# Kernel tuning notes

Measured on AMD Instinct MI355X. Metric: run time of the kernel, lower is better.

## Reference

```python
import jax, jax.numpy as jnp
import numpy as np

N = 50000
E = 800000
F_IN = 64
HID = 64


def setup_inputs() -> dict:
    key = jax.random.key(0)
    k1, k2, k3, k4, k5, k6 = jax.random.split(key, 6)
    x = jax.random.normal(k1, (N, F_IN), dtype=jnp.float32)
    edge_index = jax.random.randint(k2, (2, E), 0, N, dtype=jnp.int64)
    # GraphSAGE mean-aggregator layers: Linear(2*in -> out) applied to [x || mean_agg(x)]
    W1 = jax.random.normal(k3, (2 * F_IN, HID), dtype=jnp.float32) / np.sqrt(2 * F_IN)
    b1 = jnp.zeros((HID,), dtype=jnp.float32)
    W2 = jax.random.normal(k4, (2 * HID, HID), dtype=jnp.float32) / np.sqrt(2 * HID)
    b2 = jnp.zeros((HID,), dtype=jnp.float32)
    return {"x": x, "edge_index": edge_index, "W1": W1, "b1": b1, "W2": W2, "b2": b2}


def _sage_conv(x, src, dst, W, b):
    # mean aggregation of neighbor (src) features at dst, then linear on [self || agg]
    msg = x[src]                                                   # [E, d] gather
    s = jax.ops.segment_sum(msg, dst, num_segments=N)              # [N, d]
    cnt = jax.ops.segment_sum(jnp.ones((src.shape[0], 1), x.dtype), dst, num_segments=N)
    agg = s / jnp.maximum(cnt, 1.0)
    return jnp.concatenate([x, agg], axis=-1) @ W + b


def reference(x, edge_index, W1, b1, W2, b2):
    src, dst = edge_index[0], edge_index[1]
    h = _sage_conv(x, src, dst, W1, b1)
    h = jax.nn.relu(h)  # dropout is identity at inference
    h = _sage_conv(h, src, dst, W2, b2)
    return h
```

## Files before the change

### kernel.cpp

```cpp
#include <hip/hip_runtime.h>

#define N_NODES 50000
#define N_EDGES 800000
#define F 64
#define CHUNK 6144
#define NWG1 ((N_EDGES + CHUNK - 1) / CHUNK)
#define NBUCK 196
#define BSTRIDE 8192
#define NWTILE (N_NODES / 16)

typedef __attribute__((ext_vector_type(8))) _Float16 half8;
typedef __attribute__((ext_vector_type(4))) float f32x4;

__global__ __launch_bounds__(256) void partition_conv(
    const int*    __restrict__ src, const int* __restrict__ dst,
    const float4* __restrict__ xin,
    half8*        __restrict__ x16,
    const float*  __restrict__ W1, const float* __restrict__ W2,
    _Float16*     __restrict__ Wt1, _Float16* __restrict__ Wt2,
    unsigned*     __restrict__ bcur,
    unsigned*     __restrict__ ebuf) {
  int t = threadIdx.x, b = blockIdx.x;
  if (b == NWG1) {
    for (int i = t; i < 64 * 128; i += 256) {
      int n = i >> 7, k = i & 127;
      Wt1[i] = (_Float16)W1[k * 64 + n];
      Wt2[i] = (_Float16)W2[k * 64 + n];
    }
    return;
  }
  __shared__ int hist[256], lscan[256], lcur[256], gbase[256];
  __shared__ unsigned stage[CHUNK];
  hist[t] = 0; __syncthreads();
  int e0 = b * CHUNK;
  int cnt = N_EDGES - e0; if (cnt > CHUNK) cnt = CHUNK;
  for (int i = t; i < cnt; i += 256) atomicAdd(&hist[dst[e0 + i] >> 8], 1);

  const int TOT = N_NODES * F / 8;
  for (int i = b * 256 + t; i < TOT; i += NWG1 * 256) {
    float4 a = xin[i * 2], c = xin[i * 2 + 1];
    half8 hh;
    hh[0] = (_Float16)a.x; hh[1] = (_Float16)a.y;
    hh[2] = (_Float16)a.z; hh[3] = (_Float16)a.w;
    hh[4] = (_Float16)c.x; hh[5] = (_Float16)c.y;
    hh[6] = (_Float16)c.z; hh[7] = (_Float16)c.w;
    x16[i] = hh;
  }
  __syncthreads();

  int v = hist[t];
  lscan[t] = v; __syncthreads();
  for (int off = 1; off < 256; off <<= 1) {
    int a = (t >= off) ? lscan[t - off] : 0;
    __syncthreads();
    lscan[t] += a;
    __syncthreads();
  }
  lscan[t] -= v;
  lcur[t] = lscan[t];
  if (v > 0) gbase[t] = (int)atomicAdd(&bcur[t], (unsigned)v);
  __syncthreads();

  for (int i = t; i < cnt; i += 256) {
    int d = dst[e0 + i], s = src[e0 + i];
    int bb = d >> 8;
    int p = atomicAdd(&lcur[bb], 1);
    stage[p] = ((unsigned)bb << 24) | ((unsigned)(d & 255) << 16) | (unsigned)s;
  }
  __syncthreads();
  for (int i = t; i < cnt; i += 256) {
    unsigned e = stage[i];
    int bb = e >> 24;
    ebuf[bb * BSTRIDE + gbase[bb] + (i - lscan[bb])] = e;
  }
}

__global__ __launch_bounds__(256) void bucket_sort(
    const unsigned* __restrict__ ebuf, const unsigned* __restrict__ bcur,
    unsigned short* __restrict__ edge_src, int* __restrict__ row_start,
    int* __restrict__ deg) {
  __shared__ int lhist[256], lscan[256], lcur[256];
  __shared__ unsigned short srt[BSTRIDE];
  int b = blockIdx.x, t = threadIdx.x;
  int s0 = b * BSTRIDE;
  int cnt = (int)bcur[b];

  lhist[t] = 0; __syncthreads();
  for (int i = t; i < cnt; i += 256) atomicAdd(&lhist[(ebuf[s0 + i] >> 16) & 255], 1);
  __syncthreads();

  int v = lhist[t];
  lscan[t] = v; __syncthreads();
  for (int off = 1; off < 256; off <<= 1) {
    int a = (t >= off) ? lscan[t - off] : 0;
    __syncthreads();
    lscan[t] += a;
    __syncthreads();
  }
  lscan[t] -= v;
  lcur[t] = lscan[t];
  __syncthreads();

  for (int i = t; i < cnt; i += 256) {
    unsigned e = ebuf[s0 + i];
    int p = atomicAdd(&lcur[(e >> 16) & 255], 1);
    srt[p] = (unsigned short)(e & 0xFFFFu);
  }
  __syncthreads();

  for (int i = t; i < cnt; i += 256) edge_src[s0 + i] = srt[i];

  int n = b * 256 + t;
  if (n < N_NODES) { row_start[n] = s0 + lscan[t]; deg[n] = v; }
}

__global__ __launch_bounds__(256) void sage_layer_fused(
    const half8*    __restrict__ feat16,
    const _Float16* __restrict__ self16,
    const int*      __restrict__ row_start,
    const int*      __restrict__ deg,
    const unsigned short* __restrict__ edge_src,
    const _Float16* __restrict__ Wt,
    const float*    __restrict__ bias,
    float*          __restrict__ outf,
    unsigned short* __restrict__ out16,
    int do_relu) {
  __shared__ _Float16 lmean[32 * 72];
  int t = threadIdx.x;
  int w = t >> 6, lane = t & 63;

  {
    int o = lane >> 3, q = lane & 7;
    int n = blockIdx.x * 32 + w * 8 + o;
    if (n < N_NODES) {
      int start = row_start[n];
      int d     = deg[n];
      float a0=0.f,a1=0.f,a2=0.f,a3=0.f,a4=0.f,a5=0.f,a6=0.f,a7=0.f;
      for (int base = 0; base < d; base += 8) {
        #pragma unroll
        for (int uu = 0; uu < 8; ++uu) {
          int e = base + uu;
          if (e < d) {
            int s = (int)edge_src[start + e];
            half8 v = feat16[(size_t)s * 8 + q];
            a0 += (float)v[0]; a1 += (float)v[1]; a2 += (float)v[2]; a3 += (float)v[3];
            a4 += (float)v[4]; a5 += (float)v[5]; a6 += (float)v[6]; a7 += (float)v[7];
          }
        }
      }
      float inv = (d > 0) ? 1.0f / (float)d : 0.0f;
      half8 h;
      h[0] = (_Float16)(a0*inv); h[1] = (_Float16)(a1*inv);
      h[2] = (_Float16)(a2*inv); h[3] = (_Float16)(a3*inv);
      h[4] = (_Float16)(a4*inv); h[5] = (_Float16)(a5*inv);
      h[6] = (_Float16)(a6*inv); h[7] = (_Float16)(a7*inv);
      *(half8*)&lmean[(w * 8 + o) * 72 + q * 8] = h;
    }
  }
  __syncthreads();

  int tile = w >> 1;
  int wt = blockIdx.x * 2 + tile;
  if (wt >= NWTILE) return;
  int m = lane & 15, quad = lane >> 4;
  size_t arow = (size_t)(wt * 16 + m) * 64 + quad * 8;
  half8 a0 = *(const half8*)(self16 + arow);
  half8 a1 = *(const half8*)(self16 + arow + 32);
  int ln = tile * 16 + m;
  half8 a2 = *(const half8*)&lmean[ln * 72 + quad * 8];
  half8 a3 = *(const half8*)&lmean[ln * 72 + quad * 8 + 32];

  int nt0 = (w & 1) * 2;
  #pragma unroll
  for (int i = 0; i < 2; ++i) {
    int nt = nt0 + i;
    float bv = bias[nt * 16 + m];
    f32x4 acc = (f32x4){bv, bv, bv, bv};
    const _Float16* wrow = Wt + (size_t)(nt * 16 + m) * 128 + quad * 8;
    half8 b0 = *(const half8*)(wrow);
    half8 b1 = *(const half8*)(wrow + 32);
    half8 b2 = *(const half8*)(wrow + 64);
    half8 b3 = *(const half8*)(wrow + 96);
    acc = __builtin_amdgcn_mfma_f32_16x16x32_f16(a0, b0, acc, 0, 0, 0);
    acc = __builtin_amdgcn_mfma_f32_16x16x32_f16(a1, b1, acc, 0, 0, 0);
    acc = __builtin_amdgcn_mfma_f32_16x16x32_f16(a2, b2, acc, 0, 0, 0);
    acc = __builtin_amdgcn_mfma_f32_16x16x32_f16(a3, b3, acc, 0, 0, 0);
    #pragma unroll
    for (int r = 0; r < 4; ++r) {
      size_t off = (size_t)(wt * 16 + quad * 4 + r) * 64 + nt * 16 + m;
      float v = acc[r];
      if (do_relu) v = fmaxf(v, 0.0f);
      if (outf)  outf[off] = v;
      if (out16) { _Float16 hv = (_Float16)v; out16[off] = *(unsigned short*)&hv; }
    }
  }
}

extern "C" void kernel_launch(void* const* d_in, const int* in_sizes, int n_in,
                              void* d_out, int out_size, void* d_ws, size_t ws_size,
                              hipStream_t stream) {
  const float* x  = (const float*)d_in[0];
  const int*   ei = (const int*)d_in[1];
  const float* W1 = (const float*)d_in[2];
  const float* b1 = (const float*)d_in[3];
  const float* W2 = (const float*)d_in[4];
  const float* b2 = (const float*)d_in[5];
  float* out = (float*)d_out;

  const int* src = ei;
  const int* dst = ei + N_EDGES;

  int* wsi       = (int*)d_ws;
  unsigned* bcur = (unsigned*)wsi;
  int* deg       = wsi + 256;
  int* row_start = wsi + 50304;
  unsigned short* edge_src = (unsigned short*)(wsi + 100352);
  unsigned* ebuf = (unsigned*)(wsi + 903168);
  half8* x16     = (half8*)(wsi + 2508800);
  unsigned short* h116 = (unsigned short*)(wsi + 4108800);
  _Float16* Wt1  = (_Float16*)(wsi + 5708800);
  _Float16* Wt2  = (_Float16*)(wsi + 5712896);

  hipMemsetAsync(bcur, 0, 256 * sizeof(unsigned), stream);

  dim3 blk(256);
  partition_conv<<<NWG1 + 1, blk, 0, stream>>>(
      src, dst, (const float4*)x, x16, W1, W2, Wt1, Wt2, bcur, ebuf);
  bucket_sort<<<NBUCK, blk, 0, stream>>>(ebuf, bcur, edge_src, row_start, deg);

  dim3 grd_fused((N_NODES + 31) / 32);

  sage_layer_fused<<<grd_fused, blk, 0, stream>>>(
      x16, (const _Float16*)x16, row_start, deg, edge_src,
      Wt1, b1, nullptr, h116, 1);
  sage_layer_fused<<<grd_fused, blk, 0, stream>>>(
      (const half8*)h116, (const _Float16*)h116, row_start, deg, edge_src,
      Wt2, b2, out, nullptr, 0);
}
```

Measured before the change: 160.4 us.

## Split fp16 features into column halves and gather each half in separate passes

The fp16 feature tables are stored as two 32-column halves (lo and hi), 64 bytes per node each. The aggregation gathers all edges for the lo half, then repeats the pass for the hi half, presumably to shrink the working set per pass and improve cache hit rate on random gathers. Accumulation now happens in fp16 half4 vectors instead of fp32 scalars, which cuts conversion work but risks precision loss on high-degree nodes. The edge indices are read twice, and each gather load is narrower (8 bytes per lane instead of 16).

```diff
diff --git a/kernel.cpp b/kernel.cpp
--- a/kernel.cpp
+++ b/kernel.cpp
@@ -10,12 +10,14 @@
 #define NWTILE (N_NODES / 16)
 
 typedef __attribute__((ext_vector_type(8))) _Float16 half8;
+typedef __attribute__((ext_vector_type(4))) _Float16 half4;
 typedef __attribute__((ext_vector_type(4))) float f32x4;
 
 __global__ __launch_bounds__(256) void partition_conv(
     const int*    __restrict__ src, const int* __restrict__ dst,
     const float4* __restrict__ xin,
-    half8*        __restrict__ x16,
+    half8*        __restrict__ xlo8,
+    half8*        __restrict__ xhi8,
     const float*  __restrict__ W1, const float* __restrict__ W2,
     _Float16*     __restrict__ Wt1, _Float16* __restrict__ Wt2,
     unsigned*     __restrict__ bcur,
@@ -44,7 +46,9 @@
     hh[2] = (_Float16)a.z; hh[3] = (_Float16)a.w;
     hh[4] = (_Float16)c.x; hh[5] = (_Float16)c.y;
     hh[6] = (_Float16)c.z; hh[7] = (_Float16)c.w;
-    x16[i] = hh;
+    int node = i >> 3, part = i & 7;
+    if (part < 4) xlo8[node * 4 + part]       = hh;
+    else          xhi8[node * 4 + (part - 4)] = hh;
   }
   __syncthreads();
 
@@ -115,15 +119,18 @@
 }
 
 __global__ __launch_bounds__(256) void sage_layer_fused(
-    const half8*    __restrict__ feat16,
-    const _Float16* __restrict__ self16,
+    const half4*    __restrict__ glo,
+    const half4*    __restrict__ ghi,
+    const _Float16* __restrict__ slo,
+    const _Float16* __restrict__ shi,
     const int*      __restrict__ row_start,
     const int*      __restrict__ deg,
     const unsigned short* __restrict__ edge_src,
     const _Float16* __restrict__ Wt,
     const float*    __restrict__ bias,
     float*          __restrict__ outf,
-    unsigned short* __restrict__ out16,
+    unsigned short* __restrict__ o16lo,
+    unsigned short* __restrict__ o16hi,
     int do_relu) {
   __shared__ _Float16 lmean[32 * 72];
   int t = threadIdx.x;
@@ -135,26 +142,38 @@
     if (n < N_NODES) {
       int start = row_start[n];
       int d     = deg[n];
-      float a0=0.f,a1=0.f,a2=0.f,a3=0.f,a4=0.f,a5=0.f,a6=0.f,a7=0.f;
+      half4 aclo = (half4){0, 0, 0, 0};
+      half4 achi = (half4){0, 0, 0, 0};
       for (int base = 0; base < d; base += 8) {
         #pragma unroll
         for (int uu = 0; uu < 8; ++uu) {
           int e = base + uu;
           if (e < d) {
             int s = (int)edge_src[start + e];
-            half8 v = feat16[(size_t)s * 8 + q];
-            a0 += (float)v[0]; a1 += (float)v[1]; a2 += (float)v[2]; a3 += (float)v[3];
-            a4 += (float)v[4]; a5 += (float)v[5]; a6 += (float)v[6]; a7 += (float)v[7];
+            aclo += glo[(size_t)s * 8 + q];
           }
         }
       }
+      for (int base = 0; base < d; base += 8) {
+        #pragma unroll
+        for (int uu = 0; uu < 8; ++uu) {
+          int e = base + uu;
+          if (e < d) {
+            int s = (int)edge_src[start + e];
+            achi += ghi[(size_t)s * 8 + q];
+          }
+        }
+      }
       float inv = (d > 0) ? 1.0f / (float)d : 0.0f;
-      half8 h;
-      h[0] = (_Float16)(a0*inv); h[1] = (_Float16)(a1*inv);
-      h[2] = (_Float16)(a2*inv); h[3] = (_Float16)(a3*inv);
-      h[4] = (_Float16)(a4*inv); h[5] = (_Float16)(a5*inv);
-      h[6] = (_Float16)(a6*inv); h[7] = (_Float16)(a7*inv);
-      *(half8*)&lmean[(w * 8 + o) * 72 + q * 8] = h;
+      half4 mlo, mhi;
+      #pragma unroll
+      for (int k = 0; k < 4; ++k) {
+        mlo[k] = (_Float16)((float)aclo[k] * inv);
+        mhi[k] = (_Float16)((float)achi[k] * inv);
+      }
+      int ln = w * 8 + o;
+      *(half4*)&lmean[ln * 72 + q * 4]      = mlo;
+      *(half4*)&lmean[ln * 72 + 32 + q * 4] = mhi;
     }
   }
   __syncthreads();
@@ -163,12 +182,12 @@
   int wt = blockIdx.x * 2 + tile;
   if (wt >= NWTILE) return;
   int m = lane & 15, quad = lane >> 4;
-  size_t arow = (size_t)(wt * 16 + m) * 64 + quad * 8;
-  half8 a0 = *(const half8*)(self16 + arow);
-  half8 a1 = *(const half8*)(self16 + arow + 32);
+  size_t srow = (size_t)(wt * 16 + m) * 32 + quad * 8;
+  half8 a0 = *(const half8*)(slo + srow);
+  half8 a1 = *(const half8*)(shi + srow);
   int ln = tile * 16 + m;
   half8 a2 = *(const half8*)&lmean[ln * 72 + quad * 8];
-  half8 a3 = *(const half8*)&lmean[ln * 72 + quad * 8 + 32];
+  half8 a3 = *(const half8*)&lmean[ln * 72 + 32 + quad * 8];
 
   int nt0 = (w & 1) * 2;
   #pragma unroll
@@ -187,11 +206,17 @@
     acc = __builtin_amdgcn_mfma_f32_16x16x32_f16(a3, b3, acc, 0, 0, 0);
     #pragma unroll
     for (int r = 0; r < 4; ++r) {
-      size_t off = (size_t)(wt * 16 + quad * 4 + r) * 64 + nt * 16 + m;
+      size_t row = (size_t)(wt * 16 + quad * 4 + r);
+      int col = nt * 16 + m;
       float v = acc[r];
       if (do_relu) v = fmaxf(v, 0.0f);
-      if (outf)  outf[off] = v;
-      if (out16) { _Float16 hv = (_Float16)v; out16[off] = *(unsigned short*)&hv; }
+      if (outf) outf[row * 64 + col] = v;
+      if (o16lo) {
+        _Float16 hv = (_Float16)v;
+        unsigned short us = *(unsigned short*)&hv;
+        if (nt < 2) o16lo[row * 32 + col] = us;
+        else        o16hi[row * 32 + (col - 32)] = us;
+      }
     }
   }
 }
@@ -216,8 +241,10 @@
   int* row_start = wsi + 50304;
   unsigned short* edge_src = (unsigned short*)(wsi + 100352);
   unsigned* ebuf = (unsigned*)(wsi + 903168);
-  half8* x16     = (half8*)(wsi + 2508800);
-  unsigned short* h116 = (unsigned short*)(wsi + 4108800);
+  _Float16* xlo  = (_Float16*)(wsi + 2508800);
+  _Float16* xhi  = (_Float16*)(wsi + 3308800);
+  _Float16* h1lo = (_Float16*)(wsi + 4108800);
+  _Float16* h1hi = (_Float16*)(wsi + 4908800);
   _Float16* Wt1  = (_Float16*)(wsi + 5708800);
   _Float16* Wt2  = (_Float16*)(wsi + 5712896);
 
@@ -225,15 +252,18 @@
 
   dim3 blk(256);
   partition_conv<<<NWG1 + 1, blk, 0, stream>>>(
-      src, dst, (const float4*)x, x16, W1, W2, Wt1, Wt2, bcur, ebuf);
+      src, dst, (const float4*)x, (half8*)xlo, (half8*)xhi,
+      W1, W2, Wt1, Wt2, bcur, ebuf);
   bucket_sort<<<NBUCK, blk, 0, stream>>>(ebuf, bcur, edge_src, row_start, deg);
 
   dim3 grd_fused((N_NODES + 31) / 32);
 
   sage_layer_fused<<<grd_fused, blk, 0, stream>>>(
-      x16, (const _Float16*)x16, row_start, deg, edge_src,
-      Wt1, b1, nullptr, h116, 1);
+      (const half4*)xlo, (const half4*)xhi, xlo, xhi,
+      row_start, deg, edge_src, Wt1, b1,
+      nullptr, (unsigned short*)h1lo, (unsigned short*)h1hi, 1);
   sage_layer_fused<<<grd_fused, blk, 0, stream>>>(
-      (const half8*)h116, (const _Float16*)h116, row_start, deg, edge_src,
-      Wt2, b2, out, nullptr, 0);
-}
+      (const half4*)h1lo, (const half4*)h1hi, h1lo, h1hi,
+      row_start, deg, edge_src, Wt2, b2,
+      out, nullptr, nullptr, 0);
+}
```

Measured after the change: 180.1 us. +12.3%, slower.
